# Optimization experiments

Hardware: AMD Instinct MI355X
Metric: run time of the kernel (lower is better)

Reference implementation:

```python
import jax, jax.numpy as jnp
import numpy as np

B, Tr, P = 256, 512, 128
H, P_STD, P_STATIC, HEAD_H = 128, 32, 16, 64


def _uniform(key, shape, fan_in):
    bound = 1.0 / np.sqrt(fan_in)
    return jax.random.uniform(key, shape, jnp.float32, -bound, bound)


def setup_inputs() -> dict:
    key = jax.random.key(0)
    ks = jax.random.split(key, 16)
    X_raw = jax.random.normal(ks[0], (B, Tr, P), jnp.float32)
    M_raw = (jax.random.uniform(ks[1], (B, Tr, P)) < 0.7).astype(jnp.float32)
    DT_raw = jax.random.uniform(ks[2], (B, Tr, P), jnp.float32)
    STD_agg = jax.random.normal(ks[3], (B, 64, P_STD), jnp.float32)
    Z = jax.random.normal(ks[4], (B, P_STATIC), jnp.float32)
    idx_map = jax.random.randint(ks[5], (B, 64), -1, Tr)  # -1 marks invalid slots
    x_mean = jnp.zeros((P,), jnp.float32)  # non-trainable buffer-like param
    Wd = _uniform(ks[6], (H, P), P)
    bd = _uniform(ks[7], (H,), P)
    Wih = _uniform(ks[8], (3 * H, 2 * P), H)
    bih = _uniform(ks[9], (3 * H,), H)
    Whh = _uniform(ks[10], (3 * H, H), H)
    bhh = _uniform(ks[11], (3 * H,), H)
    W1 = _uniform(ks[12], (HEAD_H, H + P_STD + P_STATIC), H + P_STD + P_STATIC)
    b1 = _uniform(ks[13], (HEAD_H,), H + P_STD + P_STATIC)
    W2 = _uniform(ks[14], (1, HEAD_H), HEAD_H)
    return {"X_raw": X_raw, "M_raw": M_raw, "DT_raw": DT_raw, "STD_agg": STD_agg,
            "Z": Z, "idx_map": idx_map, "x_mean": x_mean, "Wd": Wd, "bd": bd,
            "Wih": Wih, "bih": bih, "Whh": Whh, "bhh": bhh,
            "W1": W1, "b1": b1, "W2": W2}


def reference(X_raw, M_raw, DT_raw, STD_agg, Z, idx_map, x_mean,
              Wd, bd, Wih, bih, Whh, bhh, W1, b1, W2):
    b, tr, p = X_raw.shape
    hdim = Whh.shape[1]

    def step(h, xs):
        x, m, dt = xs  # each [B, p]
        delta = jnp.exp(-jax.nn.softplus(dt))
        x_hat = m * x + (1 - m) * x_mean
        x_dec = m * x + (1 - m) * (delta * x_hat + (1 - delta) * x_mean)
        h_til = jnp.tanh(x_hat @ Wd.T + bd)
        h = delta * h + (1 - delta) * h_til  # requires p == hdim (as in source)
        inp = jnp.concatenate([x_dec, m], axis=-1)  # [B, 2p]
        gi = inp @ Wih.T + bih
        gh = h @ Whh.T + bhh
        gi_r, gi_z, gi_n = jnp.split(gi, 3, axis=-1)
        gh_r, gh_z, gh_n = jnp.split(gh, 3, axis=-1)
        r = jax.nn.sigmoid(gi_r + gh_r)
        z = jax.nn.sigmoid(gi_z + gh_z)
        n = jnp.tanh(gi_n + r * gh_n)
        h = (1 - z) * n + z * h
        return h, h

    h0 = jnp.zeros((b, hdim), X_raw.dtype)
    xs = (jnp.swapaxes(X_raw, 0, 1), jnp.swapaxes(M_raw, 0, 1), jnp.swapaxes(DT_raw, 0, 1))
    _, Hs = jax.lax.scan(step, h0, xs)  # [Tr, B, H]
    H_raw = jnp.swapaxes(Hs, 0, 1)  # [B, Tr, H]

    mask_sel = idx_map >= 0
    idx_safe = jnp.clip(idx_map, 0, None)
    H_agg = jnp.take_along_axis(H_raw, idx_safe[:, :, None], axis=1)
    H_agg = H_agg * mask_sel[:, :, None].astype(H_raw.dtype)  # [B, Ta, H]

    Ta = idx_map.shape[1]
    Zrep = jnp.broadcast_to(Z[:, None, :], (b, Ta, Z.shape[-1]))
    feats = jnp.concatenate([H_agg, STD_agg, Zrep], axis=-1)
    eta = (jax.nn.relu(feats @ W1.T + b1) @ W2.T)[..., 0]  # dropout is identity in eval
    return eta, H_raw, H_agg, mask_sel.astype(X_raw.dtype)
```

## Files before the change

kernel.cpp:

```cpp
#include <hip/hip_runtime.h>
#include <hip/hip_bf16.h>
#include <hip/hip_fp16.h>

#define B_    256
#define TR    512
#define P_    128
#define H_    128
#define NG    384
#define KI    256
#define TA    64
#define PSTD  32
#define PSTAT 16
#define HH    64
#define FDIM  176

#define TB    16
#define NT    (TR/TB)
#define TILE_BYTES 24576

typedef __attribute__((ext_vector_type(8))) short short8;
typedef __attribute__((ext_vector_type(4))) float f32x4;
typedef _Float16 f16;
typedef __attribute__((ext_vector_type(2))) _Float16 f16x2;

__device__ __forceinline__ float bf2f(ushort u) {
    union { uint i; float f; } v; v.i = ((uint)u) << 16; return v.f;
}
__device__ __forceinline__ ushort f2bf(float f) {
    union { float f; uint u; } v; v.f = f;
    uint u = v.u;
    uint r = (u + 0x7fffu + ((u >> 16) & 1u)) >> 16;
    return (ushort)r;
}
__device__ __forceinline__ float sigf(float x) {
    return 1.f / (1.f + __expf(-x));
}
__device__ __forceinline__ float tanhf_fast(float x) {
    float ax = fabsf(x);
    float e = __expf(-2.f * ax);
    float r = (1.f - e) / (1.f + e);
    return copysignf(r, x);
}
__device__ __forceinline__ float sigf2(float x) {
    return __builtin_amdgcn_rcpf(1.f + __expf(-x));
}
__device__ __forceinline__ float tanh2(float x) {
    return 1.f - 2.f * __builtin_amdgcn_rcpf(1.f + __expf(2.f * x));
}
__device__ __forceinline__ void bar_lds() {
    __builtin_amdgcn_sched_barrier(0);
    __asm__ volatile("s_waitcnt lgkmcnt(0)");
    __builtin_amdgcn_s_barrier();
    __builtin_amdgcn_sched_barrier(0);
}
__device__ __forceinline__ float dpp_add_xor1(float x) {
    int r = __builtin_amdgcn_mov_dpp(__float_as_int(x), 0xB1, 0xF, 0xF, true);
    return x + __int_as_float(r);
}
__device__ __forceinline__ float dpp_add_xor2(float x) {
    int r = __builtin_amdgcn_mov_dpp(__float_as_int(x), 0x4E, 0xF, 0xF, true);
    return x + __int_as_float(r);
}

__global__ __launch_bounds__(256) void k_convert(
    const float* __restrict__ Wih, const float* __restrict__ Wd,
    ushort* __restrict__ wih_b, ushort* __restrict__ wd_b)
{
    int i = blockIdx.x * 256 + threadIdx.x;
    if (i < NG * KI) wih_b[i] = f2bf(Wih[i]);
    if (i < H_ * P_) wd_b[i]  = f2bf(Wd[i]);
}

#define SA 392

__global__ __launch_bounds__(256, 2) void k_gemm(
    const float* __restrict__ X, const float* __restrict__ M,
    const float* __restrict__ DT, const float* __restrict__ xmean,
    const ushort* __restrict__ wih_b, const ushort* __restrict__ wd_b,
    const float* __restrict__ bih, const float* __restrict__ bd,
    ushort* __restrict__ gi_ws, ushort* __restrict__ htil_ws,
    float* __restrict__ delta_ws)
{
    __shared__ __align__(16) ushort sA[64 * SA];
    const int tid = threadIdx.x;
    const long r0 = (long)blockIdx.x * 64;

    #pragma unroll 4
    for (int i = 0; i < 32; ++i) {
        int idx = i * 256 + tid;
        int rl = idx >> 7, k = idx & 127;
        long g = (r0 + rl) * 128 + k;
        float x = X[g], m = M[g], dt = DT[g], xm = xmean[k];
        float delta = 1.f / (1.f + __expf(dt));
        float xh = m * x + (1.f - m) * xm;
        float xd = m * x + (1.f - m) * (delta * xh + (1.f - delta) * xm);
        sA[rl * SA + k]       = f2bf(xd);
        sA[rl * SA + 128 + k] = f2bf(m);
        sA[rl * SA + 256 + k] = f2bf(xh);
        delta_ws[g] = delta;
    }
    __syncthreads();

    const int wv   = tid >> 6;
    const int lane = tid & 63;
    const int l16  = lane & 15;
    const int q    = lane >> 4;

    f32x4 acc[4][6];
    #pragma unroll
    for (int rt = 0; rt < 4; ++rt)
        #pragma unroll
        for (int nt = 0; nt < 6; ++nt) acc[rt][nt] = (f32x4){0.f, 0.f, 0.f, 0.f};

    const int nb = 96 * wv;
    #pragma unroll
    for (int ks = 0; ks < 8; ++ks) {
        short8 a[4];
        #pragma unroll
        for (int rt = 0; rt < 4; ++rt)
            a[rt] = *(const short8*)&sA[(rt * 16 + l16) * SA + ks * 32 + q * 8];
        #pragma unroll
        for (int nt = 0; nt < 6; ++nt) {
            const short8 b = *(const short8*)&wih_b[(size_t)(nb + nt * 16 + l16) * KI + ks * 32 + q * 8];
            #pragma unroll
            for (int rt = 0; rt < 4; ++rt)
                acc[rt][nt] = __builtin_amdgcn_mfma_f32_16x16x32_bf16(a[rt], b, acc[rt][nt], 0, 0, 0);
        }
    }

    f32x4 acc2[4][2];
    #pragma unroll
    for (int rt = 0; rt < 4; ++rt)
        #pragma unroll
        for (int nt = 0; nt < 2; ++nt) acc2[rt][nt] = (f32x4){0.f, 0.f, 0.f, 0.f};

    const int nb2 = 32 * wv;
    #pragma unroll
    for (int ks = 0; ks < 4; ++ks) {
        short8 a[4];
        #pragma unroll
        for (int rt = 0; rt < 4; ++rt)
            a[rt] = *(const short8*)&sA[(rt * 16 + l16) * SA + 256 + ks * 32 + q * 8];
        #pragma unroll
        for (int nt = 0; nt < 2; ++nt) {
            const short8 b = *(const short8*)&wd_b[(size_t)(nb2 + nt * 16 + l16) * P_ + ks * 32 + q * 8];
            #pragma unroll
            for (int rt = 0; rt < 4; ++rt)
                acc2[rt][nt] = __builtin_amdgcn_mfma_f32_16x16x32_bf16(a[rt], b, acc2[rt][nt], 0, 0, 0);
        }
    }

    __syncthreads();

    ushort* sOut = sA;
    #pragma unroll
    for (int nt = 0; nt < 6; ++nt) {
        const int n = nb + nt * 16 + l16;
        const float bi = bih[n];
        #pragma unroll
        for (int rt = 0; rt < 4; ++rt) {
            #pragma unroll
            for (int reg = 0; reg < 4; ++reg) {
                int row = rt * 16 + q * 4 + reg;
                sOut[row * NG + n] = f2bf(acc[rt][nt][reg] + bi);
            }
        }
    }
    __syncthreads();

    {
        uint4* dst = (uint4*)(gi_ws + (size_t)r0 * NG);
        const uint4* src = (const uint4*)sOut;
        #pragma unroll
        for (int i = 0; i < 12; ++i) dst[tid + 256 * i] = src[tid + 256 * i];
    }
    __syncthreads();

    #pragma unroll
    for (int nt = 0; nt < 2; ++nt) {
        const int n = nb2 + nt * 16 + l16;
        const float bi = bd[n];
        #pragma unroll
        for (int rt = 0; rt < 4; ++rt) {
            #pragma unroll
            for (int reg = 0; reg < 4; ++reg) {
                int row = rt * 16 + q * 4 + reg;
                sOut[row * P_ + n] = f2bf(tanhf_fast(acc2[rt][nt][reg] + bi));
            }
        }
    }
    __syncthreads();

    {
        uint4* dst = (uint4*)(htil_ws + (size_t)r0 * P_);
        const uint4* src = (const uint4*)sOut;
        #pragma unroll
        for (int i = 0; i < 4; ++i) dst[tid + 256 * i] = src[tid + 256 * i];
    }
}

__global__ __launch_bounds__(512, 2) void k_scan(
    const ushort* __restrict__ gi_ws, const ushort* __restrict__ htil_ws,
    const float* __restrict__ delta_ws, const float* __restrict__ Whh,
    const float* __restrict__ bhh, float* __restrict__ Hraw)
{
    __shared__ __align__(16) char  s_in[2][TILE_BYTES];
    __shared__ __align__(16) uint  s_hp16[2][80];

    const int tid = threadIdx.x;
    const int b   = blockIdx.x;
    const int j   = tid >> 2;
    const int q   = tid & 3;
    const long base = (long)b * TR;

    f16x2 wh[3][16];
    #pragma unroll
    for (int g = 0; g < 3; ++g) {
        const float* wp = Whh + ((g << 7) + j) * H_ + (q << 5);
        #pragma unroll
        for (int i = 0; i < 16; ++i) {
            f16x2 v;
            v[0] = (f16)wp[2 * i];
            v[1] = (f16)wp[2 * i + 1];
            wh[g][i] = v;
        }
    }
    const float bh0 = bhh[j], bh1 = bhh[128 + j], bh2 = bhh[256 + j];

    {
        const uint4* gi4 = (const uint4*)(gi_ws   + (size_t)base * NG);
        const uint4* ht4 = (const uint4*)(htil_ws + (size_t)base * P_);
        const uint4* dl4 = (const uint4*)(delta_ws + (size_t)base * P_);
        uint4 p0 = gi4[tid];
        uint4 p1 = (tid < 256) ? gi4[512 + tid] : ht4[tid - 256];
        uint4 p2 = dl4[tid];
        uint4* d = (uint4*)s_in[0];
        d[tid] = p0; d[512 + tid] = p1; d[1024 + tid] = p2;
    }
    bar_lds();

    const int wpos = ((j >> 5) * 20 + ((j & 31) >> 1)) * 2 + (j & 1);

    int cur = 0, sb = 0;
    float h = 0.f;

    for (int tile = 0; tile < NT; ++tile) {
        uint4 p0, p1, p2;
        const int has_next = (tile + 1 < NT);
        if (has_next) {
            const long tn = base + (long)(tile + 1) * TB;
            const uint4* gi4 = (const uint4*)(gi_ws   + (size_t)tn * NG);
            const uint4* ht4 = (const uint4*)(htil_ws + (size_t)tn * P_);
            const uint4* dl4 = (const uint4*)(delta_ws + (size_t)tn * P_);
            p0 = gi4[tid];
            p1 = (tid < 256) ? gi4[512 + tid] : ht4[tid - 256];
            p2 = dl4[tid];
        }

        const ushort* sgi = (const ushort*)s_in[cur];
        const ushort* sht = (const ushort*)(s_in[cur] + 12288);
        const float*  sdl = (const float*) (s_in[cur] + 16384);

        float d_c  = sdl[j];
        float ht_c = bf2f(sht[j]);
        float gr_c = bf2f(sgi[j]);
        float gz_c = bf2f(sgi[128 + j]);
        float gn_c = bf2f(sgi[256 + j]);

        for (int ts = 0; ts < TB; ++ts) {
            float h_pre = d_c * h + (1.f - d_c) * ht_c;
            if (q == 0)
                ((f16*)s_hp16[sb])[wpos] = (f16)h_pre;
            bar_lds();

            float d_n = d_c, ht_n = ht_c, gr_n = gr_c, gz_n = gz_c, gn_n = gn_c;
            if (ts + 1 < TB) {
                d_n  = sdl[(ts + 1) * P_ + j];
                ht_n = bf2f(sht[(ts + 1) * P_ + j]);
                gr_n = bf2f(sgi[(ts + 1) * NG + j]);
                gz_n = bf2f(sgi[(ts + 1) * NG + 128 + j]);
                gn_n = bf2f(sgi[(ts + 1) * NG + 256 + j]);
            }

            const uint4* hp = (const uint4*)&s_hp16[sb][q * 20];
            float ar0 = 0.f, ar1 = 0.f, az0 = 0.f, az1 = 0.f, an0 = 0.f, an1 = 0.f;
            #pragma unroll
            for (int i = 0; i < 4; ++i) {
                uint4 hv4 = hp[i];
                uint wds[4] = {hv4.x, hv4.y, hv4.z, hv4.w};
                #pragma unroll
                for (int k2 = 0; k2 < 4; ++k2) {
                    union { uint u; f16x2 h; } cv; cv.u = wds[k2];
                    const int ii = i * 4 + k2;
                    if (ii & 1) {
                        ar1 = __builtin_amdgcn_fdot2(cv.h, wh[0][ii], ar1, false);
                        az1 = __builtin_amdgcn_fdot2(cv.h, wh[1][ii], az1, false);
                        an1 = __builtin_amdgcn_fdot2(cv.h, wh[2][ii], an1, false);
                    } else {
                        ar0 = __builtin_amdgcn_fdot2(cv.h, wh[0][ii], ar0, false);
                        az0 = __builtin_amdgcn_fdot2(cv.h, wh[1][ii], az0, false);
                        an0 = __builtin_amdgcn_fdot2(cv.h, wh[2][ii], an0, false);
                    }
                }
            }
            float sr = ar0 + ar1, sz = az0 + az1, sn = an0 + an1;
            sr = dpp_add_xor2(dpp_add_xor1(sr));
            sz = dpp_add_xor2(dpp_add_xor1(sz));
            sn = dpp_add_xor2(dpp_add_xor1(sn));

            float r = sigf2(gr_c + bh0 + sr);
            float z = sigf2(gz_c + bh1 + sz);
            float n = tanh2(gn_c + r * (bh2 + sn));
            h = (1.f - z) * n + z * h_pre;
            if (q == 0)
                Hraw[(base + (long)tile * TB + ts) * P_ + j] = h;

            d_c = d_n; ht_c = ht_n; gr_c = gr_n; gz_c = gz_n; gn_c = gn_n;
            sb ^= 1;
        }

        if (has_next) {
            uint4* d = (uint4*)s_in[cur ^ 1];
            d[tid] = p0; d[512 + tid] = p1; d[1024 + tid] = p2;
            bar_lds();
            cur ^= 1;
        }
    }
}

__global__ __launch_bounds__(256) void k_head(
    const float* __restrict__ Hraw, const float* __restrict__ STD,
    const float* __restrict__ Z, const int* __restrict__ idx_map,
    const float* __restrict__ W1, const float* __restrict__ b1,
    const float* __restrict__ W2,
    float* __restrict__ eta, float* __restrict__ Hagg,
    float* __restrict__ mask_out)
{
    __shared__ float sW1[HH * FDIM];
    __shared__ float sb1[HH], sW2[HH];
    __shared__ float spart[TA][4];

    const int tid = threadIdx.x, b = blockIdx.x;
    for (int i = tid; i < HH * FDIM; i += 256) sW1[i] = W1[i];
    if (tid < HH) { sb1[tid] = b1[tid]; sW2[tid] = W2[tid]; }
    __syncthreads();

    const int s = tid >> 2, p = tid & 3;
    const int idx = idx_map[b * TA + s];
    const int valid = idx >= 0;
    const int tt = valid ? idx : 0;
    const float* hrow = Hraw + ((long)b * TR + tt) * H_;

    float acc[16];
    #pragma unroll
    for (int uu = 0; uu < 16; ++uu) acc[uu] = sb1[p * 16 + uu];

    for (int f = 0; f < FDIM; ++f) {
        float feat;
        if (f < H_)              feat = valid ? hrow[f] : 0.f;
        else if (f < H_ + PSTD)  feat = STD[((long)b * TA + s) * PSTD + (f - H_)];
        else                     feat = Z[b * PSTAT + (f - H_ - PSTD)];
        #pragma unroll
        for (int uu = 0; uu < 16; ++uu)
            acc[uu] += feat * sW1[(p * 16 + uu) * FDIM + f];
    }

    float pe = 0.f;
    #pragma unroll
    for (int uu = 0; uu < 16; ++uu) {
        float a = acc[uu];
        pe += (a > 0.f ? a : 0.f) * sW2[p * 16 + uu];
    }
    spart[s][p] = pe;

    for (int e = 0; e < 32; ++e) {
        int ee = p * 32 + e;
        Hagg[((long)b * TA + s) * H_ + ee] = valid ? hrow[ee] : 0.f;
    }
    if (p == 0) mask_out[b * TA + s] = valid ? 1.f : 0.f;

    __syncthreads();
    if (tid < TA)
        eta[b * TA + tid] = spart[tid][0] + spart[tid][1] + spart[tid][2] + spart[tid][3];
}

extern "C" void kernel_launch(void* const* d_in, const int* in_sizes, int n_in,
                              void* d_out, int out_size, void* d_ws, size_t ws_size,
                              hipStream_t stream)
{
    const float* X     = (const float*)d_in[0];
    const float* M     = (const float*)d_in[1];
    const float* DT    = (const float*)d_in[2];
    const float* STD   = (const float*)d_in[3];
    const float* Z     = (const float*)d_in[4];
    const int*   idxm  = (const int*)  d_in[5];
    const float* xmean = (const float*)d_in[6];
    const float* Wd    = (const float*)d_in[7];
    const float* bd    = (const float*)d_in[8];
    const float* Wih   = (const float*)d_in[9];
    const float* bih   = (const float*)d_in[10];
    const float* Whh   = (const float*)d_in[11];
    const float* bhh   = (const float*)d_in[12];
    const float* W1    = (const float*)d_in[13];
    const float* b1    = (const float*)d_in[14];
    const float* W2    = (const float*)d_in[15];

    const long RROWS = (long)B_ * TR;
    char* ws = (char*)d_ws;
    size_t off = 0;
    ushort* gi_ws   = (ushort*)(ws + off); off += (size_t)RROWS * NG * 2;
    ushort* htil_ws = (ushort*)(ws + off); off += (size_t)RROWS * P_ * 2;
    float*  delta_ws= (float*) (ws + off); off += (size_t)RROWS * P_ * 4;
    ushort* wih_b   = (ushort*)(ws + off); off += (size_t)NG * KI * 2;
    ushort* wd_b    = (ushort*)(ws + off); off += (size_t)H_ * P_ * 2;

    float* out   = (float*)d_out;
    float* eta   = out;
    float* Hraw  = out + 16384;
    float* Hagg  = out + 16384 + (long)B_ * TR * H_;
    float* maskO = Hagg + (long)B_ * TA * H_;

    hipLaunchKernelGGL(k_convert, dim3(384), dim3(256), 0, stream,
                       Wih, Wd, wih_b, wd_b);
    hipLaunchKernelGGL(k_gemm, dim3(2048), dim3(256), 0, stream,
                       X, M, DT, xmean, wih_b, wd_b, bih, bd,
                       gi_ws, htil_ws, delta_ws);
    hipLaunchKernelGGL(k_scan, dim3(256), dim3(512), 0, stream,
                       gi_ws, htil_ws, delta_ws, Whh, bhh, Hraw);
    hipLaunchKernelGGL(k_head, dim3(256), dim3(256), 0, stream,
                       Hraw, STD, Z, idxm, W1, b1, W2, eta, Hagg, maskO);
}
```

Measured before the change: 689.8 us.

## Remap GRU scan to two lanes per unit with pair-interleaved gate layout

The recurrent scan kernel now uses 256 threads per batch row, with two lanes per hidden unit instead of four. Each lane holds 64 Whh columns per gate in registers, and a single DPP step finishes the reduction. The gemm kernel writes gate inputs and h-tilde with two consecutive timesteps interleaved, so one 32-bit LDS load supplies a pair of steps, and the step loop is fully unrolled in pairs with software-prefetched operands. The aim is cheaper barriers and fewer LDS loads per step, at the cost of twice the dot-product chain length per lane and fewer waves to hide latency.

Result: faster. 641.5 us (-7.0%).

```diff
diff --git a/kernel.cpp b/kernel.cpp
--- a/kernel.cpp
+++ b/kernel.cpp
@@ -32,8 +32,11 @@
     uint r = (u + 0x7fffu + ((u >> 16) & 1u)) >> 16;
     return (ushort)r;
 }
-__device__ __forceinline__ float sigf(float x) {
-    return 1.f / (1.f + __expf(-x));
+__device__ __forceinline__ float bflo(uint u) {
+    union { uint i; float f; } v; v.i = u << 16; return v.f;
+}
+__device__ __forceinline__ float bfhi(uint u) {
+    union { uint i; float f; } v; v.i = u & 0xffff0000u; return v.f;
 }
 __device__ __forceinline__ float tanhf_fast(float x) {
     float ax = fabsf(x);
@@ -55,10 +58,6 @@
 }
 __device__ __forceinline__ float dpp_add_xor1(float x) {
     int r = __builtin_amdgcn_mov_dpp(__float_as_int(x), 0xB1, 0xF, 0xF, true);
-    return x + __int_as_float(r);
-}
-__device__ __forceinline__ float dpp_add_xor2(float x) {
-    int r = __builtin_amdgcn_mov_dpp(__float_as_int(x), 0x4E, 0xF, 0xF, true);
     return x + __int_as_float(r);
 }
 
@@ -157,12 +156,13 @@
     for (int nt = 0; nt < 6; ++nt) {
         const int n = nb + nt * 16 + l16;
         const float bi = bih[n];
+        const int gpart = (n >> 7) * 256 + (n & 127) * 2;
         #pragma unroll
         for (int rt = 0; rt < 4; ++rt) {
             #pragma unroll
             for (int reg = 0; reg < 4; ++reg) {
                 int row = rt * 16 + q * 4 + reg;
-                sOut[row * NG + n] = f2bf(acc[rt][nt][reg] + bi);
+                sOut[(row >> 1) * 768 + gpart + (row & 1)] = f2bf(acc[rt][nt][reg] + bi);
             }
         }
     }
@@ -185,7 +185,7 @@
             #pragma unroll
             for (int reg = 0; reg < 4; ++reg) {
                 int row = rt * 16 + q * 4 + reg;
-                sOut[row * P_ + n] = f2bf(tanhf_fast(acc2[rt][nt][reg] + bi));
+                sOut[(row >> 1) * 256 + n * 2 + (row & 1)] = f2bf(tanhf_fast(acc2[rt][nt][reg] + bi));
             }
         }
     }
@@ -199,26 +199,83 @@
     }
 }
 
-__global__ __launch_bounds__(512, 2) void k_scan(
+#define LOADP(SFX, TP) {                                                     \
+    gr##SFX = *(const uint*)&sgi[(TP) * 768 + (j << 1)];                     \
+    gz##SFX = *(const uint*)&sgi[(TP) * 768 + 256 + (j << 1)];               \
+    gn##SFX = *(const uint*)&sgi[(TP) * 768 + 512 + (j << 1)];               \
+    ht##SFX = *(const uint*)&sht[(TP) * 256 + (j << 1)];                     \
+    dl##SFX##0 = sdl[(TP) * 256 + j];                                        \
+    dl##SFX##1 = sdl[(TP) * 256 + 128 + j];                                  \
+}
+
+#define SCANSTEP(TS, SFX, PH) {                                              \
+    float d_c  = PH ? dl##SFX##1 : dl##SFX##0;                               \
+    float ht_c = PH ? bfhi(ht##SFX) : bflo(ht##SFX);                         \
+    float h_pre = d_c * h + (1.f - d_c) * ht_c;                              \
+    if (q == 0) ((f16*)s_hp16[sb])[j] = (f16)h_pre;                          \
+    bar_lds();                                                               \
+    const uint4* hp = (const uint4*)((const char*)s_hp16[sb] + q * 128);     \
+    float ar0 = 0.f, ar1 = 0.f, az0 = 0.f, az1 = 0.f, an0 = 0.f, an1 = 0.f;  \
+    _Pragma("unroll")                                                        \
+    for (int r8 = 0; r8 < 8; ++r8) {                                         \
+        uint4 hv4 = hp[r8];                                                  \
+        uint wds[4] = {hv4.x, hv4.y, hv4.z, hv4.w};                          \
+        _Pragma("unroll")                                                    \
+        for (int c = 0; c < 4; ++c) {                                        \
+            union { uint u; f16x2 h; } cv; cv.u = wds[c];                    \
+            const int ii = r8 * 4 + c;                                       \
+            if (ii & 1) {                                                    \
+                ar1 = __builtin_amdgcn_fdot2(cv.h, wh[0][ii], ar1, false);   \
+                az1 = __builtin_amdgcn_fdot2(cv.h, wh[1][ii], az1, false);   \
+                an1 = __builtin_amdgcn_fdot2(cv.h, wh[2][ii], an1, false);   \
+            } else {                                                         \
+                ar0 = __builtin_amdgcn_fdot2(cv.h, wh[0][ii], ar0, false);   \
+                az0 = __builtin_amdgcn_fdot2(cv.h, wh[1][ii], az0, false);   \
+                an0 = __builtin_amdgcn_fdot2(cv.h, wh[2][ii], an0, false);   \
+            }                                                                \
+        }                                                                    \
+    }                                                                        \
+    float sr = dpp_add_xor1(ar0 + ar1);                                      \
+    float sz = dpp_add_xor1(az0 + az1);                                      \
+    float sn = dpp_add_xor1(an0 + an1);                                      \
+    float gr_c = PH ? bfhi(gr##SFX) : bflo(gr##SFX);                         \
+    float gz_c = PH ? bfhi(gz##SFX) : bflo(gz##SFX);                         \
+    float gn_c = PH ? bfhi(gn##SFX) : bflo(gn##SFX);                         \
+    float r = sigf2(gr_c + bh0 + sr);                                        \
+    float z = sigf2(gz_c + bh1 + sz);                                        \
+    float n = tanh2(gn_c + r * (bh2 + sn));                                  \
+    h = (1.f - z) * n + z * h_pre;                                           \
+    if (q == 0)                                                              \
+        Hraw[(base + (long)tile * TB + (TS)) * P_ + j] = h;                  \
+    sb ^= 1;                                                                 \
+}
+
+#define PAIRSTEP(TP, CURS, NXTS) {                                           \
+    SCANSTEP(2 * (TP), CURS, 0);                                             \
+    if ((TP) < 7) LOADP(NXTS, (TP) + 1);                                     \
+    SCANSTEP(2 * (TP) + 1, CURS, 1);                                         \
+}
+
+__global__ __launch_bounds__(256, 1) void k_scan(
     const ushort* __restrict__ gi_ws, const ushort* __restrict__ htil_ws,
     const float* __restrict__ delta_ws, const float* __restrict__ Whh,
     const float* __restrict__ bhh, float* __restrict__ Hraw)
 {
-    __shared__ __align__(16) char  s_in[2][TILE_BYTES];
-    __shared__ __align__(16) uint  s_hp16[2][80];
+    __shared__ __align__(16) char s_in[2][TILE_BYTES];
+    __shared__ __align__(16) uint s_hp16[2][68];
 
     const int tid = threadIdx.x;
     const int b   = blockIdx.x;
-    const int j   = tid >> 2;
-    const int q   = tid & 3;
+    const int j   = tid >> 1;
+    const int q   = tid & 1;
     const long base = (long)b * TR;
 
-    f16x2 wh[3][16];
+    f16x2 wh[3][32];
     #pragma unroll
     for (int g = 0; g < 3; ++g) {
-        const float* wp = Whh + ((g << 7) + j) * H_ + (q << 5);
-        #pragma unroll
-        for (int i = 0; i < 16; ++i) {
+        const float* wp = Whh + ((g << 7) + j) * H_ + (q << 6);
+        #pragma unroll
+        for (int i = 0; i < 32; ++i) {
             f16x2 v;
             v[0] = (f16)wp[2 * i];
             v[1] = (f16)wp[2 * i + 1];
@@ -231,97 +288,50 @@
         const uint4* gi4 = (const uint4*)(gi_ws   + (size_t)base * NG);
         const uint4* ht4 = (const uint4*)(htil_ws + (size_t)base * P_);
         const uint4* dl4 = (const uint4*)(delta_ws + (size_t)base * P_);
-        uint4 p0 = gi4[tid];
-        uint4 p1 = (tid < 256) ? gi4[512 + tid] : ht4[tid - 256];
-        uint4 p2 = dl4[tid];
+        uint4 p0 = gi4[tid], p1 = gi4[256 + tid], p2 = gi4[512 + tid];
+        uint4 p3 = ht4[tid], p4 = dl4[tid], p5 = dl4[256 + tid];
         uint4* d = (uint4*)s_in[0];
-        d[tid] = p0; d[512 + tid] = p1; d[1024 + tid] = p2;
+        d[tid] = p0; d[256 + tid] = p1; d[512 + tid] = p2;
+        d[768 + tid] = p3; d[1024 + tid] = p4; d[1280 + tid] = p5;
     }
     bar_lds();
-
-    const int wpos = ((j >> 5) * 20 + ((j & 31) >> 1)) * 2 + (j & 1);
 
     int cur = 0, sb = 0;
     float h = 0.f;
 
     for (int tile = 0; tile < NT; ++tile) {
-        uint4 p0, p1, p2;
+        uint4 p0, p1, p2, p3, p4, p5;
         const int has_next = (tile + 1 < NT);
         if (has_next) {
             const long tn = base + (long)(tile + 1) * TB;
             const uint4* gi4 = (const uint4*)(gi_ws   + (size_t)tn * NG);
             const uint4* ht4 = (const uint4*)(htil_ws + (size_t)tn * P_);
             const uint4* dl4 = (const uint4*)(delta_ws + (size_t)tn * P_);
-            p0 = gi4[tid];
-            p1 = (tid < 256) ? gi4[512 + tid] : ht4[tid - 256];
-            p2 = dl4[tid];
+            p0 = gi4[tid]; p1 = gi4[256 + tid]; p2 = gi4[512 + tid];
+            p3 = ht4[tid]; p4 = dl4[tid]; p5 = dl4[256 + tid];
         }
 
         const ushort* sgi = (const ushort*)s_in[cur];
         const ushort* sht = (const ushort*)(s_in[cur] + 12288);
         const float*  sdl = (const float*) (s_in[cur] + 16384);
 
-        float d_c  = sdl[j];
-        float ht_c = bf2f(sht[j]);
-        float gr_c = bf2f(sgi[j]);
-        float gz_c = bf2f(sgi[128 + j]);
-        float gn_c = bf2f(sgi[256 + j]);
-
-        for (int ts = 0; ts < TB; ++ts) {
-            float h_pre = d_c * h + (1.f - d_c) * ht_c;
-            if (q == 0)
-                ((f16*)s_hp16[sb])[wpos] = (f16)h_pre;
-            bar_lds();
-
-            float d_n = d_c, ht_n = ht_c, gr_n = gr_c, gz_n = gz_c, gn_n = gn_c;
-            if (ts + 1 < TB) {
-                d_n  = sdl[(ts + 1) * P_ + j];
-                ht_n = bf2f(sht[(ts + 1) * P_ + j]);
-                gr_n = bf2f(sgi[(ts + 1) * NG + j]);
-                gz_n = bf2f(sgi[(ts + 1) * NG + 128 + j]);
-                gn_n = bf2f(sgi[(ts + 1) * NG + 256 + j]);
-            }
-
-            const uint4* hp = (const uint4*)&s_hp16[sb][q * 20];
-            float ar0 = 0.f, ar1 = 0.f, az0 = 0.f, az1 = 0.f, an0 = 0.f, an1 = 0.f;
-            #pragma unroll
-            for (int i = 0; i < 4; ++i) {
-                uint4 hv4 = hp[i];
-                uint wds[4] = {hv4.x, hv4.y, hv4.z, hv4.w};
-                #pragma unroll
-                for (int k2 = 0; k2 < 4; ++k2) {
-                    union { uint u; f16x2 h; } cv; cv.u = wds[k2];
-                    const int ii = i * 4 + k2;
-                    if (ii & 1) {
-                        ar1 = __builtin_amdgcn_fdot2(cv.h, wh[0][ii], ar1, false);
-                        az1 = __builtin_amdgcn_fdot2(cv.h, wh[1][ii], az1, false);
-                        an1 = __builtin_amdgcn_fdot2(cv.h, wh[2][ii], an1, false);
-                    } else {
-                        ar0 = __builtin_amdgcn_fdot2(cv.h, wh[0][ii], ar0, false);
-                        az0 = __builtin_amdgcn_fdot2(cv.h, wh[1][ii], az0, false);
-                        an0 = __builtin_amdgcn_fdot2(cv.h, wh[2][ii], an0, false);
-                    }
-                }
-            }
-            float sr = ar0 + ar1, sz = az0 + az1, sn = an0 + an1;
-            sr = dpp_add_xor2(dpp_add_xor1(sr));
-            sz = dpp_add_xor2(dpp_add_xor1(sz));
-            sn = dpp_add_xor2(dpp_add_xor1(sn));
-
-            float r = sigf2(gr_c + bh0 + sr);
-            float z = sigf2(gz_c + bh1 + sz);
-            float n = tanh2(gn_c + r * (bh2 + sn));
-            h = (1.f - z) * n + z * h_pre;
-            if (q == 0)
-                Hraw[(base + (long)tile * TB + ts) * P_ + j] = h;
-
-            d_c = d_n; ht_c = ht_n; gr_c = gr_n; gz_c = gz_n; gn_c = gn_n;
-            sb ^= 1;
-        }
+        uint grA, gzA, gnA, htA; float dlA0, dlA1;
+        uint grB, gzB, gnB, htB; float dlB0, dlB1;
+        LOADP(A, 0);
+
+        PAIRSTEP(0, A, B);
+        PAIRSTEP(1, B, A);
+        PAIRSTEP(2, A, B);
+        PAIRSTEP(3, B, A);
+        PAIRSTEP(4, A, B);
+        PAIRSTEP(5, B, A);
+        PAIRSTEP(6, A, B);
+        PAIRSTEP(7, B, A);
 
         if (has_next) {
             uint4* d = (uint4*)s_in[cur ^ 1];
-            d[tid] = p0; d[512 + tid] = p1; d[1024 + tid] = p2;
+            d[tid] = p0; d[256 + tid] = p1; d[512 + tid] = p2;
+            d[768 + tid] = p3; d[1024 + tid] = p4; d[1280 + tid] = p5;
             bar_lds();
             cur ^= 1;
         }
@@ -425,7 +435,7 @@
     hipLaunchKernelGGL(k_gemm, dim3(2048), dim3(256), 0, stream,
                        X, M, DT, xmean, wih_b, wd_b, bih, bd,
                        gi_ws, htil_ws, delta_ws);
-    hipLaunchKernelGGL(k_scan, dim3(256), dim3(512), 0, stream,
+    hipLaunchKernelGGL(k_scan, dim3(256), dim3(256), 0, stream,
                        gi_ws, htil_ws, delta_ws, Whh, bhh, Hraw);
     hipLaunchKernelGGL(k_head, dim3(256), dim3(256), 0, stream,
                        Hraw, STD, Z, idxm, W1, b1, W2, eta, Hagg, maskO);
```
